# Kernel tuning notes

Hardware: AMD Instinct MI355X
Metric: run time of the kernel (lower is better)

Reference implementation:

```python
import jax, jax.numpy as jnp
import numpy as np

BETA_MIN, BETA_MAX = 0.01, 0.995
EPS_DELTA, EPS_RMS = 1e-6, 1e-5


def _rmsnorm(x, w):
    ms = jnp.mean(x * x, axis=-1, keepdims=True)
    return x * jax.lax.rsqrt(ms + EPS_RMS) * w


def _delta_scan(q, k, v, beta, mask, bb1, bb2):
    # q, k, v: [B, S, D]; beta, mask: [B, S, 1]; bb1, bb2: scalars
    phi_q = jax.nn.elu(q) + 1.0
    phi_k = jax.nn.elu(k) + 1.0
    b1_base = jnp.clip(jax.nn.sigmoid(bb1), BETA_MIN, BETA_MAX)
    b2_base = jnp.clip(jax.nn.sigmoid(bb2), BETA_MIN, BETA_MAX)
    B, S, D = q.shape

    def step(carry, inp):
        H1, H2, Z1, Z2 = carry
        qt, kt, vt, bt, mt = inp  # qt/kt/vt: [B,D], bt/mt: [B,1]
        bin_t = jnp.clip(bt, BETA_MIN, BETA_MAX)
        b1 = jnp.clip(b1_base * bin_t, BETA_MIN, BETA_MAX)  # [B,1]
        b2 = jnp.clip(b2_base * bin_t, BETA_MIN, BETA_MAX)
        kv = jnp.einsum('bd,be->bde', kt, vt) * mt[:, :, None]  # [B,D,D]
        H1 = H1 * b1[:, :, None] + kv
        H2 = H2 * b2[:, :, None] + kv
        km = kt * mt
        Z1 = Z1 * b1 + km
        Z2 = Z2 * b2 + km
        num = jnp.einsum('bd,bde->be', qt, H1 + H2)
        den = jnp.maximum(jnp.sum(qt * (Z1 + Z2), axis=-1, keepdims=True), EPS_DELTA)
        return (H1, H2, Z1, Z2), num / den * mt

    init = (jnp.zeros((B, D, D), q.dtype), jnp.zeros((B, D, D), q.dtype),
            jnp.zeros((B, D), q.dtype), jnp.zeros((B, D), q.dtype))
    xs = tuple(a.swapaxes(0, 1) for a in (phi_q, phi_k, v, beta, mask))
    _, outs = jax.lax.scan(step, init, xs)
    return outs.swapaxes(0, 1)  # [B, S, D]


def setup_inputs() -> dict:
    key = jax.random.key(0)
    B, S, Dm, H = 4, 2048, 512, 8
    ks = jax.random.split(key, 8)
    scale = float(1.0 / np.sqrt(Dm))
    return {
        'x': jax.random.normal(ks[0], (B, S, Dm), jnp.float32),
        'mask': jnp.ones((B, S), jnp.float32),
        'Wq': jax.random.normal(ks[1], (Dm, Dm), jnp.float32) * scale,
        'Wk': jax.random.normal(ks[2], (Dm, Dm), jnp.float32) * scale,
        'Wv': jax.random.normal(ks[3], (Dm, Dm), jnp.float32) * scale,
        'Wb': jax.random.normal(ks[4], (H, Dm), jnp.float32) * scale,
        'bb': jnp.full((H,), 1.5, jnp.float32),
        'Wo': jax.random.normal(ks[5], (Dm, Dm), jnp.float32) * scale,
        'bo': jnp.zeros((Dm,), jnp.float32),
        'ln_w': jnp.ones((Dm,), jnp.float32),
        'recency': jnp.zeros((H,), jnp.float32),
        'base_beta_1': jnp.asarray(2.0, jnp.float32),
        'base_beta_2': jnp.asarray(3.0, jnp.float32),
    }


def reference(x, mask, Wq, Wk, Wv, Wb, bb, Wo, bo, ln_w, recency,
              base_beta_1, base_beta_2):
    B, S, Dm = x.shape
    H = recency.shape[0]
    d = Dm // H
    h = _rmsnorm(x, ln_w)
    q = h @ Wq.T
    k = h @ Wk.T
    v = h @ Wv.T
    # input-conditioned gate with per-head recency bias  -> [B, S, H]
    beta = jax.nn.sigmoid(h @ Wb.T + bb + recency)

    def to_heads(t):  # [B,S,Dm] -> [B*H, S, d]
        return t.reshape(B, S, H, d).transpose(0, 2, 1, 3).reshape(B * H, S, d)

    qh, kh, vh = to_heads(q), to_heads(k), to_heads(v)
    betah = beta.transpose(0, 2, 1).reshape(B * H, S, 1)
    maskh = jnp.broadcast_to(mask[:, None, :, None], (B, H, S, 1)).reshape(B * H, S, 1)
    o = _delta_scan(qh, kh, vh, betah, maskh, base_beta_1, base_beta_2)
    o = o.reshape(B, H, S, d).transpose(0, 2, 1, 3).reshape(B, S, Dm)
    return x + (o @ Wo.T + bo)
```

## Files before the change

### kernel.cpp

```cpp
#include <hip/hip_runtime.h>
#include <stdint.h>

typedef unsigned short u16;
typedef short bf16x8 __attribute__((ext_vector_type(8)));
typedef unsigned short u16x8 __attribute__((ext_vector_type(8)));
typedef unsigned short u16x4 __attribute__((ext_vector_type(4)));
typedef float f32x4 __attribute__((ext_vector_type(4)));

#define S_ 2048
#define DM 512
#define DH 64
#define CL 64
#define NCH 32

#define SW(r, sc) ((r) * 72 + ((sc) ^ (((r) & 7) << 3)))

__device__ __forceinline__ float b2f(u16 u) { return __uint_as_float(((unsigned)u) << 16); }
__device__ __forceinline__ u16 f2b(float f) {
    unsigned v = __float_as_uint(f);
    unsigned r = v + 0x7fffu + ((v >> 16) & 1u);
    return (u16)(r >> 16);
}
__device__ __forceinline__ float phi_elu(float x) { return x > 0.f ? x + 1.f : __expf(x); }
__device__ __forceinline__ float clip01(float v) { return fminf(fmaxf(v, 0.01f), 0.995f); }

__device__ __forceinline__ void gload16(const u16* g, u16* l) {
    __builtin_amdgcn_global_load_lds((const __attribute__((address_space(1))) void*)g,
                                     (__attribute__((address_space(3))) void*)l, 16, 0, 0);
}

__global__ __launch_bounds__(256) void k_rb(const float* __restrict__ x, const float* __restrict__ lnw,
                                            const float* __restrict__ Wb, const float* __restrict__ bb,
                                            const float* __restrict__ rec, const float* __restrict__ bb1p,
                                            const float* __restrict__ bb2p, u16* __restrict__ h,
                                            float* __restrict__ lb1, float* __restrict__ lb2) {
    int wave = threadIdx.x >> 6, lane = threadIdx.x & 63;
    int row = blockIdx.x * 4 + wave;
    const float* xr = x + (size_t)row * DM + lane * 8;
    float4 v0 = *(const float4*)xr;
    float4 v1 = *(const float4*)(xr + 4);
    float ss = v0.x * v0.x + v0.y * v0.y + v0.z * v0.z + v0.w * v0.w +
               v1.x * v1.x + v1.y * v1.y + v1.z * v1.z + v1.w * v1.w;
    #pragma unroll
    for (int off = 32; off; off >>= 1) ss += __shfl_xor(ss, off, 64);
    float sc = rsqrtf(ss * (1.f / DM) + 1e-5f);
    const float* wr_ = lnw + lane * 8;
    float4 w0 = *(const float4*)wr_;
    float4 w1 = *(const float4*)(wr_ + 4);
    float hv[8];
    hv[0] = v0.x * sc * w0.x; hv[1] = v0.y * sc * w0.y;
    hv[2] = v0.z * sc * w0.z; hv[3] = v0.w * sc * w0.w;
    hv[4] = v1.x * sc * w1.x; hv[5] = v1.y * sc * w1.y;
    hv[6] = v1.z * sc * w1.z; hv[7] = v1.w * sc * w1.w;
    u16x8 o;
    #pragma unroll
    for (int j = 0; j < 8; j++) o[j] = f2b(hv[j]);
    *(u16x8*)(h + (size_t)row * DM + lane * 8) = o;
    float acc[8];
    #pragma unroll
    for (int hd = 0; hd < 8; hd++) {
        const float* wp = Wb + hd * DM + lane * 8;
        float4 a0 = *(const float4*)wp;
        float4 a1 = *(const float4*)(wp + 4);
        acc[hd] = hv[0] * a0.x + hv[1] * a0.y + hv[2] * a0.z + hv[3] * a0.w +
                  hv[4] * a1.x + hv[5] * a1.y + hv[6] * a1.z + hv[7] * a1.w;
    }
    #pragma unroll
    for (int hd = 0; hd < 8; hd++) {
        #pragma unroll
        for (int off = 32; off; off >>= 1) acc[hd] += __shfl_xor(acc[hd], off, 64);
    }
    if (lane == 0) {
        float b1b = clip01(1.f / (1.f + __expf(-bb1p[0])));
        float b2b = clip01(1.f / (1.f + __expf(-bb2p[0])));
        int b = row >> 11, s = row & 2047;
        #pragma unroll
        for (int hd = 0; hd < 8; hd++) {
            float logit = acc[hd] + bb[hd] + rec[hd];
            float beta = 1.f / (1.f + __expf(-logit));
            float bin = clip01(beta);
            float b1 = clip01(b1b * bin);
            float b2 = clip01(b2b * bin);
            size_t o2 = (size_t)((b << 3) + hd) * S_ + s;
            lb1[o2] = log2f(b1);
            lb2[o2] = log2f(b2);
        }
    }
}

__global__ __launch_bounds__(256) void k_convw(const float* __restrict__ Wq, const float* __restrict__ Wk,
                                               const float* __restrict__ Wv, const float* __restrict__ Wo,
                                               u16* __restrict__ wcat, u16* __restrict__ wo) {
    int idx = blockIdx.x * 256 + threadIdx.x;
    int e0 = idx << 2;
    if (e0 < 1536 * 512) {
        int r = e0 >> 9, ccol = e0 & 511;
        const float* src = (r < 512) ? (Wq + (size_t)r * 512)
                         : (r < 1024) ? (Wk + (size_t)(r - 512) * 512)
                                      : (Wv + (size_t)(r - 1024) * 512);
        float4 v = *(const float4*)(src + ccol);
        u16x4 o = {f2b(v.x), f2b(v.y), f2b(v.z), f2b(v.w)};
        *(u16x4*)(wcat + e0) = o;
    } else {
        int e = e0 - 1536 * 512;
        float4 v = *(const float4*)(Wo + e);
        u16x4 o = {f2b(v.x), f2b(v.y), f2b(v.z), f2b(v.w)};
        *(u16x4*)(wo + e) = o;
    }
}

template<int MODE, int NT>
__global__ __launch_bounds__(256) void k_gemm(const u16* __restrict__ A, const u16* __restrict__ Bw, int K,
                                              const float* __restrict__ mask, u16* __restrict__ qh,
                                              u16* __restrict__ kh, u16* __restrict__ vh,
                                              const float* __restrict__ xres, const float* __restrict__ bo,
                                              float* __restrict__ outp) {
    __shared__ u16 As[128 * 32];
    __shared__ u16 Bs[128 * 32];
    int tid = threadIdx.x;
    int lane = tid & 63, w = tid >> 6;
    int wr = w >> 1, wc = w & 1;
    int hwid = blockIdx.y * gridDim.x + blockIdx.x;
    int nwg = gridDim.x * NT;
    int q8 = nwg >> 3;
    int logical = (hwid & 7) * q8 + (hwid >> 3);
    int mTile = logical / NT, nTile = logical % NT;
    int m0 = mTile * 128, n0 = nTile * 128;
    f32x4 acc[4][4] = {};
    int srow = w * 32 + (lane >> 2);
    int skel = (lane & 3) << 3;
    const u16* gA0 = A + (size_t)(m0 + srow) * K + skel;
    const u16* gA1 = gA0 + (size_t)16 * K;
    const u16* gB0 = Bw + (size_t)(n0 + srow) * K + skel;
    const u16* gB1 = gB0 + (size_t)16 * K;
    u16* lA0 = &As[(w * 32) * 32];
    u16* lA1 = &As[(w * 32 + 16) * 32];
    u16* lB0 = &Bs[(w * 32) * 32];
    u16* lB1 = &Bs[(w * 32 + 16) * 32];
    int l15 = lane & 15, kh8 = (lane >> 4) << 3;
    for (int k0 = 0; k0 < K; k0 += 32) {
        if (k0) __syncthreads();
        gload16(gA0 + k0, lA0);
        gload16(gA1 + k0, lA1);
        gload16(gB0 + k0, lB0);
        gload16(gB1 + k0, lB1);
        __syncthreads();
        bf16x8 af[4], bfr[4];
        #pragma unroll
        for (int m = 0; m < 4; m++) af[m] = *(const bf16x8*)&As[(wr * 64 + m * 16 + l15) * 32 + kh8];
        #pragma unroll
        for (int n = 0; n < 4; n++) bfr[n] = *(const bf16x8*)&Bs[(wc * 64 + n * 16 + l15) * 32 + kh8];
        #pragma unroll
        for (int m = 0; m < 4; m++)
            #pragma unroll
            for (int n = 0; n < 4; n++)
                acc[m][n] = __builtin_amdgcn_mfma_f32_16x16x32_bf16(af[m], bfr[n], acc[m][n], 0, 0, 0);
    }
    #pragma unroll
    for (int m = 0; m < 4; m++) {
        int rbase = m0 + wr * 64 + m * 16 + ((lane >> 4) << 2);
        #pragma unroll
        for (int n = 0; n < 4; n++) {
            int col = n0 + wc * 64 + n * 16 + l15;
            #pragma unroll
            for (int r = 0; r < 4; r++) {
                int row = rbase + r;
                float v = acc[m][n][r];
                if constexpr (MODE == 0) {
                    int mat = col >> 9, f = col & 511, hh = f >> 6, j = f & 63;
                    int b = row >> 11, s = row & 2047;
                    size_t di = ((size_t)((b << 3) + hh) * S_ + s) * DH + j;
                    if (mat == 0) qh[di] = f2b(phi_elu(v));
                    else if (mat == 1) kh[di] = f2b(phi_elu(v) * mask[(b << 11) + s]);
                    else vh[di] = f2b(v);
                } else {
                    size_t oi = (size_t)row * DM + col;
                    outp[oi] = v + xres[oi] + bo[col];
                }
            }
        }
    }
}

__global__ __launch_bounds__(256) void k_pass1(const u16* __restrict__ kh, const u16* __restrict__ vh,
                                               const float* __restrict__ lb1, const float* __restrict__ lb2,
                                               u16* __restrict__ S1b, u16* __restrict__ S2b,
                                               float* __restrict__ z1, float* __restrict__ z2,
                                               float* __restrict__ P1, float* __restrict__ P2) {
    __shared__ u16 Kw1[64 * 72];
    __shared__ u16 Kw2[64 * 72];
    __shared__ u16 Vt[64 * 72];
    __shared__ float Ls1[64], Ls2[64];
    int tid = threadIdx.x;
    int bh = blockIdx.x >> 5, c = blockIdx.x & 31;
    int wave = tid >> 6, lane = tid & 63;
    size_t base = ((size_t)bh * S_ + c * CL) * DH;
    if (wave == 0) {
        float v = lb1[(size_t)bh * S_ + c * CL + lane];
        #pragma unroll
        for (int d = 1; d < 64; d <<= 1) { float o = __shfl_up(v, d, 64); if (lane >= d) v += o; }
        Ls1[lane] = v;
    } else if (wave == 1) {
        float v = lb2[(size_t)bh * S_ + c * CL + lane];
        #pragma unroll
        for (int d = 1; d < 64; d <<= 1) { float o = __shfl_up(v, d, 64); if (lane >= d) v += o; }
        Ls2[lane] = v;
    }
    int ss = tid & 63, i0 = (tid >> 6) << 4;
    const u16* kr = kh + base + (size_t)ss * DH + i0;
    u16x8 kk0 = *(const u16x8*)kr;
    u16x8 kk1 = *(const u16x8*)(kr + 8);
    {
        const u16* vr = vh + base + (size_t)ss * DH + i0;
        u16x8 vv0 = *(const u16x8*)vr;
        u16x8 vv1 = *(const u16x8*)(vr + 8);
        #pragma unroll
        for (int j = 0; j < 8; j++) {
            Vt[SW(i0 + j, ss)] = vv0[j];
            Vt[SW(i0 + 8 + j, ss)] = vv1[j];
        }
    }
    __syncthreads();
    float w1 = exp2f(Ls1[63] - Ls1[ss]);
    float w2 = exp2f(Ls2[63] - Ls2[ss]);
    #pragma unroll
    for (int j = 0; j < 8; j++) {
        float k0 = b2f(kk0[j]), k1 = b2f(kk1[j]);
        Kw1[SW(i0 + j, ss)] = f2b(w1 * k0);
        Kw2[SW(i0 + j, ss)] = f2b(w2 * k0);
        Kw1[SW(i0 + 8 + j, ss)] = f2b(w1 * k1);
        Kw2[SW(i0 + 8 + j, ss)] = f2b(w2 * k1);
    }
    if (tid == 0) { P1[blockIdx.x] = exp2f(Ls1[63]); P2[blockIdx.x] = exp2f(Ls2[63]); }
    __syncthreads();
    int l15 = lane & 15, kh8 = (lane >> 4) << 3;
    int j0 = wave << 4;
    bf16x8 vf0 = *(const bf16x8*)&Vt[SW(j0 + l15, kh8)];
    bf16x8 vf1 = *(const bf16x8*)&Vt[SW(j0 + l15, 32 + kh8)];
    f32x4 a1[4], a2[4];
    #pragma unroll
    for (int it = 0; it < 4; it++) { a1[it] = (f32x4){0,0,0,0}; a2[it] = (f32x4){0,0,0,0}; }
    #pragma unroll
    for (int it = 0; it < 4; it++) {
        int ir = (it << 4) + l15;
        bf16x8 b0 = *(const bf16x8*)&Kw1[SW(ir, kh8)];
        bf16x8 b1 = *(const bf16x8*)&Kw1[SW(ir, 32 + kh8)];
        a1[it] = __builtin_amdgcn_mfma_f32_16x16x32_bf16(vf0, b0, a1[it], 0, 0, 0);
        a1[it] = __builtin_amdgcn_mfma_f32_16x16x32_bf16(vf1, b1, a1[it], 0, 0, 0);
        bf16x8 c0 = *(const bf16x8*)&Kw2[SW(ir, kh8)];
        bf16x8 c1 = *(const bf16x8*)&Kw2[SW(ir, 32 + kh8)];
        a2[it] = __builtin_amdgcn_mfma_f32_16x16x32_bf16(vf0, c0, a2[it], 0, 0, 0);
        a2[it] = __builtin_amdgcn_mfma_f32_16x16x32_bf16(vf1, c1, a2[it], 0, 0, 0);
    }
    {
        int iz = tid >> 2, sg = tid & 3;
        u16x8 x0 = *(const u16x8*)&Kw1[SW(iz, sg << 4)];
        u16x8 x1 = *(const u16x8*)&Kw1[SW(iz, (sg << 4) + 8)];
        u16x8 y0 = *(const u16x8*)&Kw2[SW(iz, sg << 4)];
        u16x8 y1 = *(const u16x8*)&Kw2[SW(iz, (sg << 4) + 8)];
        float z1v = 0.f, z2v = 0.f;
        #pragma unroll
        for (int j = 0; j < 8; j++) {
            z1v += b2f(x0[j]) + b2f(x1[j]);
            z2v += b2f(y0[j]) + b2f(y1[j]);
        }
        z1v += __shfl_xor(z1v, 1, 64); z1v += __shfl_xor(z1v, 2, 64);
        z2v += __shfl_xor(z2v, 1, 64); z2v += __shfl_xor(z2v, 2, 64);
        if (sg == 0) {
            z1[(size_t)blockIdx.x * 64 + iz] = z1v;
            z2[(size_t)blockIdx.x * 64 + iz] = z2v;
        }
    }
    int jr0 = j0 + ((lane >> 4) << 2);
    size_t so = (size_t)blockIdx.x * 4096;
    #pragma unroll
    for (int it = 0; it < 4; it++) {
        int ii = (it << 4) + l15;
        #pragma unroll
        for (int r = 0; r < 4; r++) {
            S1b[so + (size_t)(jr0 + r) * 64 + ii] = f2b(a1[it][r]);
            S2b[so + (size_t)(jr0 + r) * 64 + ii] = f2b(a2[it][r]);
        }
    }
}

__global__ __launch_bounds__(256) void k_pass2(u16* __restrict__ S1b, u16* __restrict__ S2b,
                                               float* __restrict__ z1, float* __restrict__ z2,
                                               const float* __restrict__ P1, const float* __restrict__ P2) {
    int blk = blockIdx.x;
    if (blk < 512) {
        int bh = blk >> 4;
        int e = ((blk & 15) << 8) + threadIdx.x;
        float c1 = 0.f, c2 = 0.f;
        #pragma unroll 4
        for (int c = 0; c < NCH; c++) {
            int bc = bh * NCH + c;
            size_t idx = (size_t)bc * 4096 + e;
            float p1 = P1[bc], p2 = P2[bc];
            float t1 = b2f(S1b[idx]); S1b[idx] = f2b(c1); c1 = c1 * p1 + t1;
            float t2 = b2f(S2b[idx]); S2b[idx] = f2b(c2); c2 = c2 * p2 + t2;
        }
    } else {
        int bh = ((blk - 512) << 2) + (threadIdx.x >> 6);
        int e = threadIdx.x & 63;
        float y1 = 0.f, y2 = 0.f;
        #pragma unroll 4
        for (int c = 0; c < NCH; c++) {
            int bc = bh * NCH + c;
            size_t zi = (size_t)bc * 64 + e;
            float p1 = P1[bc], p2 = P2[bc];
            float t1 = z1[zi]; z1[zi] = y1; y1 = y1 * p1 + t1;
            float t2 = z2[zi]; z2[zi] = y2; y2 = y2 * p2 + t2;
        }
    }
}

__global__ __launch_bounds__(256) void k_pass3(const u16* __restrict__ qh, const u16* __restrict__ kh,
                                               const u16* __restrict__ vh, const float* __restrict__ lb1,
                                               const float* __restrict__ lb2, const u16* __restrict__ S1b,
                                               const u16* __restrict__ S2b, const float* __restrict__ z1,
                                               const float* __restrict__ z2, const float* __restrict__ mask,
                                               u16* __restrict__ obf) {
    __shared__ u16 Vt[64 * 72];
    __shared__ u16 AWs[64 * 72];
    __shared__ float Ls1[64], Ls2[64], dens[64], qZ1[64], qZ2[64];
    int tid = threadIdx.x;
    int bh = blockIdx.x >> 5, c = blockIdx.x & 31;
    int wave = tid >> 6, lane = tid & 63;
    size_t base = ((size_t)bh * S_ + c * CL) * DH;
    if (wave == 0) {
        float v = lb1[(size_t)bh * S_ + c * CL + lane];
        #pragma unroll
        for (int d = 1; d < 64; d <<= 1) { float o = __shfl_up(v, d, 64); if (lane >= d) v += o; }
        Ls1[lane] = v;
    } else if (wave == 1) {
        float v = lb2[(size_t)bh * S_ + c * CL + lane];
        #pragma unroll
        for (int d = 1; d < 64; d <<= 1) { float o = __shfl_up(v, d, 64); if (lane >= d) v += o; }
        Ls2[lane] = v;
    }
    {
        int ss = tid & 63, i0 = (tid >> 6) << 4;
        const u16* vr = vh + base + (size_t)ss * DH + i0;
        u16x8 vv0 = *(const u16x8*)vr;
        u16x8 vv1 = *(const u16x8*)(vr + 8);
        #pragma unroll
        for (int j = 0; j < 8; j++) {
            Vt[SW(i0 + j, ss)] = vv0[j];
            Vt[SW(i0 + 8 + j, ss)] = vv1[j];
        }
    }
    {
        int t = tid >> 2, g = tid & 3;
        const u16* qp = qh + base + (size_t)t * DH + (g << 4);
        u16x8 q0 = *(const u16x8*)qp;
        u16x8 q1 = *(const u16x8*)(qp + 8);
        const float* z1p = z1 + (size_t)blockIdx.x * 64 + (g << 4);
        const float* z2p = z2 + (size_t)blockIdx.x * 64 + (g << 4);
        float az1 = 0.f, az2 = 0.f;
        #pragma unroll
        for (int m = 0; m < 8; m++) {
            float qv0 = b2f(q0[m]), qv1 = b2f(q1[m]);
            az1 += qv0 * z1p[m] + qv1 * z1p[m + 8];
            az2 += qv0 * z2p[m] + qv1 * z2p[m + 8];
        }
        az1 += __shfl_xor(az1, 1, 64); az1 += __shfl_xor(az1, 2, 64);
        az2 += __shfl_xor(az2, 1, 64); az2 += __shfl_xor(az2, 2, 64);
        if (g == 0) { qZ1[t] = az1; qZ2[t] = az2; }
    }
    int l15 = lane & 15, kh8 = (lane >> 4) << 3;
    int t0 = wave << 4;
    const u16* qb = qh + base + (size_t)(t0 + l15) * DH;
    bf16x8 qf0 = *(const bf16x8*)(qb + kh8);
    bf16x8 qf1 = *(const bf16x8*)(qb + 32 + kh8);
    f32x4 accA[4];
    #pragma unroll
    for (int st = 0; st < 4; st++) accA[st] = (f32x4){0, 0, 0, 0};
    #pragma unroll
    for (int st = 0; st < 4; st++) {
        const u16* kb = kh + base + (size_t)((st << 4) + l15) * DH;
        bf16x8 kf0 = *(const bf16x8*)(kb + kh8);
        bf16x8 kf1 = *(const bf16x8*)(kb + 32 + kh8);
        accA[st] = __builtin_amdgcn_mfma_f32_16x16x32_bf16(qf0, kf0, accA[st], 0, 0, 0);
        accA[st] = __builtin_amdgcn_mfma_f32_16x16x32_bf16(qf1, kf1, accA[st], 0, 0, 0);
    }
    __syncthreads();
    int trow = t0 + ((lane >> 4) << 2);
    float l1t[4], l2t[4];
    #pragma unroll
    for (int r = 0; r < 4; r++) { l1t[r] = Ls1[trow + r]; l2t[r] = Ls2[trow + r]; }
    float rs[4] = {0.f, 0.f, 0.f, 0.f};
    #pragma unroll
    for (int st = 0; st < 4; st++) {
        int s = (st << 4) + l15;
        float s1 = Ls1[s], s2 = Ls2[s];
        #pragma unroll
        for (int r = 0; r < 4; r++) {
            float w = 0.f;
            if (s <= trow + r) w = exp2f(l1t[r] - s1) + exp2f(l2t[r] - s2);
            u16 awb = f2b(accA[st][r] * w);
            AWs[SW(trow + r, s)] = awb;
            rs[r] += b2f(awb);
        }
    }
    #pragma unroll
    for (int off = 1; off < 16; off <<= 1) {
        #pragma unroll
        for (int r = 0; r < 4; r++) rs[r] += __shfl_xor(rs[r], off, 64);
    }
    if (l15 == 0) {
        #pragma unroll
        for (int r = 0; r < 4; r++) dens[trow + r] = rs[r];
    }
    __syncthreads();
    bf16x8 awf0 = *(const bf16x8*)&AWs[SW(t0 + l15, kh8)];
    bf16x8 awf1 = *(const bf16x8*)&AWs[SW(t0 + l15, 32 + kh8)];
    const u16* h1g = S1b + (size_t)blockIdx.x * 4096;
    const u16* h2g = S2b + (size_t)blockIdx.x * 4096;
    f32x4 accO[4], accC1[4], accC2[4];
    #pragma unroll
    for (int jt = 0; jt < 4; jt++) {
        accO[jt] = (f32x4){0, 0, 0, 0};
        accC1[jt] = (f32x4){0, 0, 0, 0};
        accC2[jt] = (f32x4){0, 0, 0, 0};
    }
    #pragma unroll
    for (int jt = 0; jt < 4; jt++) {
        int jr = (jt << 4) + l15;
        bf16x8 v0 = *(const bf16x8*)&Vt[SW(jr, kh8)];
        bf16x8 v1 = *(const bf16x8*)&Vt[SW(jr, 32 + kh8)];
        accO[jt] = __builtin_amdgcn_mfma_f32_16x16x32_bf16(awf0, v0, accO[jt], 0, 0, 0);
        accO[jt] = __builtin_amdgcn_mfma_f32_16x16x32_bf16(awf1, v1, accO[jt], 0, 0, 0);
        bf16x8 h10 = *(const bf16x8*)(h1g + (size_t)jr * 64 + kh8);
        bf16x8 h11 = *(const bf16x8*)(h1g + (size_t)jr * 64 + 32 + kh8);
        accC1[jt] = __builtin_amdgcn_mfma_f32_16x16x32_bf16(qf0, h10, accC1[jt], 0, 0, 0);
        accC1[jt] = __builtin_amdgcn_mfma_f32_16x16x32_bf16(qf1, h11, accC1[jt], 0, 0, 0);
        bf16x8 h20 = *(const bf16x8*)(h2g + (size_t)jr * 64 + kh8);
        bf16x8 h21 = *(const bf16x8*)(h2g + (size_t)jr * 64 + 32 + kh8);
        accC2[jt] = __builtin_amdgcn_mfma_f32_16x16x32_bf16(qf0, h20, accC2[jt], 0, 0, 0);
        accC2[jt] = __builtin_amdgcn_mfma_f32_16x16x32_bf16(qf1, h21, accC2[jt], 0, 0, 0);
    }
    int b = bh >> 3, hh = bh & 7;
    #pragma unroll
    for (int r = 0; r < 4; r++) {
        int t = trow + r;
        float e1 = exp2f(l1t[r]), e2 = exp2f(l2t[r]);
        float den = dens[t] + e1 * qZ1[t] + e2 * qZ2[t];
        den = fmaxf(den, 1e-6f);
        int sg = (c << 6) + t;
        float mv = mask[(size_t)b * S_ + sg];
        float inv = mv / den;
        u16* op = obf + ((size_t)b * S_ + sg) * DM + hh * DH;
        #pragma unroll
        for (int jt = 0; jt < 4; jt++) {
            float numv = accO[jt][r] + e1 * accC1[jt][r] + e2 * accC2[jt][r];
            op[(jt << 4) + l15] = f2b(numv * inv);
        }
    }
}

extern "C" void kernel_launch(void* const* d_in, const int* in_sizes, int n_in,
                              void* d_out, int out_size, void* d_ws, size_t ws_size,
                              hipStream_t stream) {
    const float* x    = (const float*)d_in[0];
    const float* mask = (const float*)d_in[1];
    const float* Wq   = (const float*)d_in[2];
    const float* Wk   = (const float*)d_in[3];
    const float* Wv   = (const float*)d_in[4];
    const float* Wb   = (const float*)d_in[5];
    const float* bb   = (const float*)d_in[6];
    const float* Wo   = (const float*)d_in[7];
    const float* bo   = (const float*)d_in[8];
    const float* lnw  = (const float*)d_in[9];
    const float* rec  = (const float*)d_in[10];
    const float* bb1  = (const float*)d_in[11];
    const float* bb2  = (const float*)d_in[12];
    float* out = (float*)d_out;

    char* w = (char*)d_ws;
    u16* h    = (u16*)w;  w += (size_t)8192 * 512 * 2;
    u16* wcat = (u16*)w;  w += (size_t)1536 * 512 * 2;
    u16* wo   = (u16*)w;  w += (size_t)512 * 512 * 2;
    u16* qh   = (u16*)w;  w += (size_t)8192 * 512 * 2;
    u16* kh   = (u16*)w;  w += (size_t)8192 * 512 * 2;
    u16* vh   = (u16*)w;  w += (size_t)8192 * 512 * 2;
    float* lb1 = (float*)w; w += (size_t)32 * 2048 * 4;
    float* lb2 = (float*)w; w += (size_t)32 * 2048 * 4;
    u16* S1b  = (u16*)w;  w += (size_t)1024 * 4096 * 2;
    u16* S2b  = (u16*)w;  w += (size_t)1024 * 4096 * 2;
    float* z1  = (float*)w; w += (size_t)1024 * 64 * 4;
    float* z2  = (float*)w; w += (size_t)1024 * 64 * 4;
    float* P1  = (float*)w; w += 4096;
    float* P2  = (float*)w; w += 4096;
    u16* obf   = (u16*)w;   w += (size_t)8192 * 512 * 2;

    k_rb<<<2048, 256, 0, stream>>>(x, lnw, Wb, bb, rec, bb1, bb2, h, lb1, lb2);
    k_convw<<<1024, 256, 0, stream>>>(Wq, Wk, Wv, Wo, wcat, wo);
    k_gemm<0, 12><<<dim3(64, 12), 256, 0, stream>>>(h, wcat, 512, mask, qh, kh, vh, nullptr, nullptr, nullptr);
    k_pass1<<<1024, 256, 0, stream>>>(kh, vh, lb1, lb2, S1b, S2b, z1, z2, P1, P2);
    k_pass2<<<520, 256, 0, stream>>>(S1b, S2b, z1, z2, P1, P2);
    k_pass3<<<1024, 256, 0, stream>>>(qh, kh, vh, lb1, lb2, S1b, S2b, z1, z2, mask, obf);
    k_gemm<1, 4><<<dim3(64, 4), 256, 0, stream>>>(obf, wo, 512, nullptr, nullptr, nullptr, nullptr, x, bo, out);
}
```

Before: 112.3 us.

## Stage GEMM epilogues through LDS for vectorized stores and merge weight-convert kernel

The GEMM epilogues now write accumulators into shared memory and then emit coalesced 16-byte stores. The QKV path writes 8 bf16 per store into the head-major layout, and the output path reads the residual and bias as float4 and writes float4. This replaces scattered 2-byte and 4-byte per-element global stores. Separately, the weight bf16 conversion is folded into the RMSnorm/beta kernel as extra blocks, removing one launch. In exchange the epilogue adds several __syncthreads and extra LDS traffic, and shared memory grows to about 17.5 KB.

```diff
diff --git a/kernel.cpp b/kernel.cpp
--- a/kernel.cpp
+++ b/kernel.cpp
@@ -29,11 +29,33 @@
                                      (__attribute__((address_space(3))) void*)l, 16, 0, 0);
 }
 
-__global__ __launch_bounds__(256) void k_rb(const float* __restrict__ x, const float* __restrict__ lnw,
-                                            const float* __restrict__ Wb, const float* __restrict__ bb,
-                                            const float* __restrict__ rec, const float* __restrict__ bb1p,
-                                            const float* __restrict__ bb2p, u16* __restrict__ h,
-                                            float* __restrict__ lb1, float* __restrict__ lb2) {
+__global__ __launch_bounds__(256) void k_rbw(const float* __restrict__ x, const float* __restrict__ lnw,
+                                             const float* __restrict__ Wb, const float* __restrict__ bb,
+                                             const float* __restrict__ rec, const float* __restrict__ bb1p,
+                                             const float* __restrict__ bb2p, u16* __restrict__ h,
+                                             float* __restrict__ lb1, float* __restrict__ lb2,
+                                             const float* __restrict__ Wq, const float* __restrict__ Wk,
+                                             const float* __restrict__ Wv, const float* __restrict__ Wo,
+                                             u16* __restrict__ wcat, u16* __restrict__ wo) {
+    if (blockIdx.x >= 2048) {
+        int idx = (blockIdx.x - 2048) * 256 + threadIdx.x;
+        int e0 = idx << 2;
+        if (e0 < 1536 * 512) {
+            int r = e0 >> 9, ccol = e0 & 511;
+            const float* src = (r < 512) ? (Wq + (size_t)r * 512)
+                             : (r < 1024) ? (Wk + (size_t)(r - 512) * 512)
+                                          : (Wv + (size_t)(r - 1024) * 512);
+            float4 v = *(const float4*)(src + ccol);
+            u16x4 o = {f2b(v.x), f2b(v.y), f2b(v.z), f2b(v.w)};
+            *(u16x4*)(wcat + e0) = o;
+        } else {
+            int e = e0 - 1536 * 512;
+            float4 v = *(const float4*)(Wo + e);
+            u16x4 o = {f2b(v.x), f2b(v.y), f2b(v.z), f2b(v.w)};
+            *(u16x4*)(wo + e) = o;
+        }
+        return;
+    }
     int wave = threadIdx.x >> 6, lane = threadIdx.x & 63;
     int row = blockIdx.x * 4 + wave;
     const float* xr = x + (size_t)row * DM + lane * 8;
@@ -88,35 +110,15 @@
     }
 }
 
-__global__ __launch_bounds__(256) void k_convw(const float* __restrict__ Wq, const float* __restrict__ Wk,
-                                               const float* __restrict__ Wv, const float* __restrict__ Wo,
-                                               u16* __restrict__ wcat, u16* __restrict__ wo) {
-    int idx = blockIdx.x * 256 + threadIdx.x;
-    int e0 = idx << 2;
-    if (e0 < 1536 * 512) {
-        int r = e0 >> 9, ccol = e0 & 511;
-        const float* src = (r < 512) ? (Wq + (size_t)r * 512)
-                         : (r < 1024) ? (Wk + (size_t)(r - 512) * 512)
-                                      : (Wv + (size_t)(r - 1024) * 512);
-        float4 v = *(const float4*)(src + ccol);
-        u16x4 o = {f2b(v.x), f2b(v.y), f2b(v.z), f2b(v.w)};
-        *(u16x4*)(wcat + e0) = o;
-    } else {
-        int e = e0 - 1536 * 512;
-        float4 v = *(const float4*)(Wo + e);
-        u16x4 o = {f2b(v.x), f2b(v.y), f2b(v.z), f2b(v.w)};
-        *(u16x4*)(wo + e) = o;
-    }
-}
-
 template<int MODE, int NT>
 __global__ __launch_bounds__(256) void k_gemm(const u16* __restrict__ A, const u16* __restrict__ Bw, int K,
                                               const float* __restrict__ mask, u16* __restrict__ qh,
                                               u16* __restrict__ kh, u16* __restrict__ vh,
                                               const float* __restrict__ xres, const float* __restrict__ bo,
                                               float* __restrict__ outp) {
-    __shared__ u16 As[128 * 32];
-    __shared__ u16 Bs[128 * 32];
+    __shared__ u16 SH[8960];
+    u16* As = SH;
+    u16* Bs = SH + 4096;
     int tid = threadIdx.x;
     int lane = tid & 63, w = tid >> 6;
     int wr = w >> 1, wc = w & 1;
@@ -156,28 +158,89 @@
             for (int n = 0; n < 4; n++)
                 acc[m][n] = __builtin_amdgcn_mfma_f32_16x16x32_bf16(af[m], bfr[n], acc[m][n], 0, 0, 0);
     }
-    #pragma unroll
-    for (int m = 0; m < 4; m++) {
-        int rbase = m0 + wr * 64 + m * 16 + ((lane >> 4) << 2);
-        #pragma unroll
-        for (int n = 0; n < 4; n++) {
-            int col = n0 + wc * 64 + n * 16 + l15;
-            #pragma unroll
-            for (int r = 0; r < 4; r++) {
-                int row = rbase + r;
-                float v = acc[m][n][r];
-                if constexpr (MODE == 0) {
-                    int mat = col >> 9, f = col & 511, hh = f >> 6, j = f & 63;
-                    int b = row >> 11, s = row & 2047;
-                    size_t di = ((size_t)((b << 3) + hh) * S_ + s) * DH + j;
-                    if (mat == 0) qh[di] = f2b(phi_elu(v));
-                    else if (mat == 1) kh[di] = f2b(phi_elu(v) * mask[(b << 11) + s]);
-                    else vh[di] = f2b(v);
-                } else {
-                    size_t oi = (size_t)row * DM + col;
-                    outp[oi] = v + xres[oi] + bo[col];
+    __syncthreads();
+    if constexpr (MODE == 0) {
+        int mat = n0 >> 9;
+        int cb = n0 & 511;
+        u16* basep = (mat == 0) ? qh : (mat == 1) ? kh : vh;
+        #pragma unroll
+        for (int P = 0; P < 2; P++) {
+            if (wr == P) {
+                #pragma unroll
+                for (int m = 0; m < 4; m++)
+                    #pragma unroll
+                    for (int n = 0; n < 4; n++)
+                        #pragma unroll
+                        for (int r = 0; r < 4; r++) {
+                            int rl = m * 16 + ((lane >> 4) << 2) + r;
+                            int colL = wc * 64 + n * 16 + l15;
+                            SH[rl * 140 + colL] = f2b(acc[m][n][r]);
+                        }
+            }
+            __syncthreads();
+            {
+                int rl = tid >> 2;
+                int gr = m0 + P * 64 + rl;
+                int b = gr >> 11, s = gr & 2047;
+                float mv = (mat == 1) ? mask[(b << 11) + s] : 1.f;
+                #pragma unroll
+                for (int cc = 0; cc < 4; cc++) {
+                    int cl = ((tid & 3) << 5) + (cc << 3);
+                    u16x8 vv = *(const u16x8*)&SH[rl * 140 + cl];
+                    int f = cb + cl;
+                    int hh = f >> 6, j = f & 63;
+                    u16* dst = basep + ((size_t)(b * 8 + hh) * S_ + s) * DH + j;
+                    if (mat == 2) {
+                        *(u16x8*)dst = vv;
+                    } else {
+                        u16x8 ov;
+                        #pragma unroll
+                        for (int e = 0; e < 8; e++) {
+                            float v = b2f(vv[e]);
+                            ov[e] = f2b(phi_elu(v) * mv);
+                        }
+                        *(u16x8*)dst = ov;
+                    }
                 }
             }
+            __syncthreads();
+        }
+    } else {
+        float* SF = (float*)SH;
+        #pragma unroll
+        for (int Pq = 0; Pq < 4; Pq++) {
+            if (wr == (Pq >> 1)) {
+                int mbase = (Pq & 1) * 2;
+                #pragma unroll
+                for (int mm = 0; mm < 2; mm++)
+                    #pragma unroll
+                    for (int n = 0; n < 4; n++)
+                        #pragma unroll
+                        for (int r = 0; r < 4; r++) {
+                            int rl = mm * 16 + ((lane >> 4) << 2) + r;
+                            int colL = wc * 64 + n * 16 + l15;
+                            SF[rl * 136 + colL] = acc[mbase + mm][n][r];
+                        }
+            }
+            __syncthreads();
+            {
+                int rl = tid >> 3;
+                int gr = m0 + Pq * 32 + rl;
+                int col0 = (tid & 7) << 4;
+                const float* xr = xres + (size_t)gr * DM + n0 + col0;
+                float* orow = outp + (size_t)gr * DM + n0 + col0;
+                #pragma unroll
+                for (int cc = 0; cc < 4; cc++) {
+                    int cl = col0 + (cc << 2);
+                    float4 v = *(const float4*)&SF[rl * 136 + cl];
+                    float4 xv = *(const float4*)(xr + (cc << 2));
+                    float4 bv = *(const float4*)(bo + n0 + cl);
+                    float4 ov = {v.x + xv.x + bv.x, v.y + xv.y + bv.y,
+                                 v.z + xv.z + bv.z, v.w + xv.w + bv.w};
+                    *(float4*)(orow + (cc << 2)) = ov;
+                }
+            }
+            __syncthreads();
         }
     }
 }
@@ -494,8 +557,8 @@
     float* P2  = (float*)w; w += 4096;
     u16* obf   = (u16*)w;   w += (size_t)8192 * 512 * 2;
 
-    k_rb<<<2048, 256, 0, stream>>>(x, lnw, Wb, bb, rec, bb1, bb2, h, lb1, lb2);
-    k_convw<<<1024, 256, 0, stream>>>(Wq, Wk, Wv, Wo, wcat, wo);
+    k_rbw<<<3072, 256, 0, stream>>>(x, lnw, Wb, bb, rec, bb1, bb2, h, lb1, lb2,
+                                    Wq, Wk, Wv, Wo, wcat, wo);
     k_gemm<0, 12><<<dim3(64, 12), 256, 0, stream>>>(h, wcat, 512, mask, qh, kh, vh, nullptr, nullptr, nullptr);
     k_pass1<<<1024, 256, 0, stream>>>(kh, vh, lb1, lb2, S1b, S2b, z1, z2, P1, P2);
     k_pass2<<<520, 256, 0, stream>>>(S1b, S2b, z1, z2, P1, P2);
```

New measurement: 105.0 us. -6.6%, faster.
